# Performance work log

Hardware: AMD Instinct MI355X
Metric: run time of the kernel (lower is better)

Reference implementation:

```python
import jax, jax.numpy as jnp
import numpy as np

B, S, DM, H, DK, R, THETA = 8, 2048, 512, 8, 64, 128, 10000.0
BLK = R          # key/query block size; window radius == block size
NB = S // BLK    # number of blocks
NEG = -1e30      # additive mask for invalid positions (fp32-safe)


def setup_inputs() -> dict:
    key = jax.random.key(0)
    ks = jax.random.split(key, 5)
    scale = 0.02
    hidden_states = jax.random.normal(ks[0], (B, S, DM), jnp.float32)
    Wq = jax.random.normal(ks[1], (DM, H * DK), jnp.float32) * scale
    Wk = jax.random.normal(ks[2], (DM, H * DK), jnp.float32) * scale
    Wv = jax.random.normal(ks[3], (DM, H * DK), jnp.float32) * scale
    Wo = jax.random.normal(ks[4], (H * DK, DM), jnp.float32) * scale
    position_ids = jnp.tile(jnp.arange(S, dtype=jnp.int64)[None, :], (B, 1))
    return {"hidden_states": hidden_states, "Wq": Wq, "Wk": Wk, "Wv": Wv,
            "Wo": Wo, "position_ids": position_ids}


def _apply_rope(q, k, position_ids):
    # q,k: [B,H,S,DK]; position_ids: [B,S]
    half = DK // 2
    inv_freq = 1.0 / (THETA ** (jnp.arange(0, DK, 2, dtype=jnp.float32) / DK))  # [half]
    freqs = position_ids.astype(jnp.float32)[:, :, None] * inv_freq[None, None, :]  # [B,S,half]
    emb = jnp.concatenate([freqs, freqs], axis=-1)        # [B,S,DK]
    cos = jnp.cos(emb)[:, None, :, :]                     # [B,1,S,DK]
    sin = jnp.sin(emb)[:, None, :, :]

    def rotate_half(x):
        return jnp.concatenate([-x[..., half:], x[..., :half]], axis=-1)

    return q * cos + rotate_half(q) * sin, k * cos + rotate_half(k) * sin


def _band_mask():
    # valid[nb, BLK, 3*BLK]: key within [0,S) and |j - i| <= R
    b = jnp.arange(NB)[:, None, None]
    qi = jnp.arange(BLK)[None, :, None]
    kj = jnp.arange(3 * BLK)[None, None, :]
    kglob = (b - 1) * BLK + kj                 # global key index
    qglob = b * BLK + qi                        # global query index
    return (jnp.abs(kglob - qglob) <= R) & (kglob >= 0) & (kglob < S)


def reference(hidden_states, Wq, Wk, Wv, Wo, position_ids):
    # projections: [B,S,DM] -> [B,H,S,DK]
    def shape(x):
        return x.reshape(B, S, H, DK).transpose(0, 2, 1, 3)

    q = shape(hidden_states @ Wq)
    k = shape(hidden_states @ Wk)
    v = shape(hidden_states @ Wv)
    q, k = _apply_rope(q, k, position_ids)

    # block-banded sliding-window attention, softmax_scale = 1.0 (no scaling)
    pad = ((0, 0), (0, 0), (BLK, BLK), (0, 0))
    kb = jnp.pad(k, pad).reshape(B, H, NB + 2, BLK, DK)
    vb = jnp.pad(v, pad).reshape(B, H, NB + 2, BLK, DK)
    # neighbor window: blocks [b-1, b, b+1] -> [B,H,NB,3*BLK,DK]
    kwin = jnp.concatenate([kb[:, :, i:i + NB] for i in range(3)], axis=3)
    vwin = jnp.concatenate([vb[:, :, i:i + NB] for i in range(3)], axis=3)
    qb = q.reshape(B, H, NB, BLK, DK)

    scores = jnp.einsum('bhnqd,bhnkd->bhnqk', qb, kwin)   # unscaled
    valid = _band_mask()                                  # [NB,BLK,3*BLK]
    scores = jnp.where(valid[None, None], scores, NEG)
    attn = jax.nn.softmax(scores.astype(jnp.float32), axis=-1).astype(scores.dtype)
    outb = jnp.einsum('bhnqk,bhnkd->bhnqd', attn, vwin)   # [B,H,NB,BLK,DK]

    out = outb.reshape(B, H, S, DK).transpose(0, 2, 1, 3).reshape(B, S, H * DK)
    return out @ Wo
```

## Files before the change

### kernel.cpp

```cpp
#include <hip/hip_runtime.h>

using bf16 = __bf16;
typedef __bf16 bf16x8 __attribute__((ext_vector_type(8)));
typedef __bf16 bf16x4 __attribute__((ext_vector_type(4)));
typedef float f32x4 __attribute__((ext_vector_type(4)));
typedef float f32x16 __attribute__((ext_vector_type(16)));

#define MFMA16(a, b, c) __builtin_amdgcn_mfma_f32_16x16x32_bf16((a), (b), (c), 0, 0, 0)
#define MFMA32(a, b, c) __builtin_amdgcn_mfma_f32_32x32x16_bf16((a), (b), (c), 0, 0, 0)

constexpr int S = 2048, DM = 512, H = 8, DK = 64, HD = 512;
constexpr int NBLK = 16, BLK = 128;
constexpr int Mrows = 8 * S;
constexpr float LOG2E = 1.44269504088896340736f;

__device__ __forceinline__ void gll16(const void* g, void* l) {
  __builtin_amdgcn_global_load_lds((const __attribute__((address_space(1))) unsigned int*)g,
                                   (__attribute__((address_space(3))) unsigned int*)l, 16, 0, 0);
}

__global__ void k_conv(const float* __restrict__ x, bf16* __restrict__ y) {
  size_t i = ((size_t)blockIdx.x * 256 + threadIdx.x) * 8;
  float4 a = *(const float4*)(x + i);
  float4 b = *(const float4*)(x + i + 4);
  bf16x8 o;
  o[0] = (bf16)a.x; o[1] = (bf16)a.y; o[2] = (bf16)a.z; o[3] = (bf16)a.w;
  o[4] = (bf16)b.x; o[5] = (bf16)b.y; o[6] = (bf16)b.z; o[7] = (bf16)b.w;
  *(bf16x8*)(y + i) = o;
}

__global__ void k_transw4(const float* __restrict__ W0, const float* __restrict__ W1,
                          const float* __restrict__ W2, const float* __restrict__ W3,
                          bf16* __restrict__ D0, bf16* __restrict__ D1,
                          bf16* __restrict__ D2, bf16* __restrict__ D3) {
  const int z = blockIdx.z;
  const float* W = (z == 0) ? W0 : (z == 1) ? W1 : (z == 2) ? W2 : W3;
  bf16* Wt = (z == 0) ? D0 : (z == 1) ? D1 : (z == 2) ? D2 : D3;
  __shared__ float tile[32][33];
  int k0 = blockIdx.x * 32, n0 = blockIdx.y * 32;
  int tx = threadIdx.x, ty = threadIdx.y;
#pragma unroll
  for (int i = 0; i < 4; i++)
    tile[ty * 4 + i][tx] = W[(size_t)(k0 + ty * 4 + i) * 512 + n0 + tx];
  __syncthreads();
#pragma unroll
  for (int i = 0; i < 4; i++)
    Wt[(size_t)(n0 + ty * 4 + i) * 512 + k0 + tx] = (bf16)tile[tx][ty * 4 + i];
}

__global__ void k_ctab(float2* __restrict__ ctab) {
  int idx = blockIdx.x * 256 + threadIdx.x;
  int s = idx >> 5, i = idx & 31;
  float invf = exp2f(-(float)i * (13.287712379549449f / 32.0f));
  float ang = (float)s * invf;
  ctab[idx] = make_float2(cosf(ang), sinf(ang));
}

__global__ __launch_bounds__(256) void k_gemm_qkv(
    const bf16* __restrict__ Xb,
    const bf16* __restrict__ Wtq, const bf16* __restrict__ Wtk, const bf16* __restrict__ Wtv,
    bf16* __restrict__ Qo, bf16* __restrict__ Ko, bf16* __restrict__ Vt,
    const float2* __restrict__ ctab) {
  const int bid = blockIdx.x;
  const int xcd = bid & 7, i = bid >> 3;
  const int mloc = i / 12, zy = i % 12;
  const int z = zy >> 2, y = zy & 3;
  const bf16* Wt = (z == 0) ? Wtq : ((z == 1) ? Wtk : Wtv);
  bf16* dst = (z == 0) ? Qo : Ko;
  const float qscale = (z == 0) ? LOG2E : 1.0f;

  __shared__ __align__(16) char Asm2[2][8192];
  __shared__ __align__(16) char Bsm2[2][8192];

  const int t = threadIdx.x, l = t & 63, wid = t >> 6;
  const int l15 = l & 15, l4 = l >> 4;
  const int wm = wid >> 1, wn = wid & 1;
  const size_t arow0 = (size_t)(xcd * 16 + mloc) * 128;
  const size_t brow0 = (size_t)y * 128;

  f32x4 acc[4][4] = {};
  const int rs = wid * 16 + (l >> 2);
  const int cs = (l & 3) ^ ((l >> 2) & 3);

  auto stage = [&](int kt, int b) {
    const int k0 = kt * 32;
    gll16(Xb + (arow0 + rs) * 512 + k0 + cs * 8,      Asm2[b] + wid * 1024);
    gll16(Xb + (arow0 + 64 + rs) * 512 + k0 + cs * 8, Asm2[b] + 4096 + wid * 1024);
    gll16(Wt + (brow0 + rs) * 512 + k0 + cs * 8,      Bsm2[b] + wid * 1024);
    gll16(Wt + (brow0 + 64 + rs) * 512 + k0 + cs * 8, Bsm2[b] + 4096 + wid * 1024);
  };

  stage(0, 0);
  asm volatile("s_waitcnt vmcnt(0)" ::: "memory");
  __builtin_amdgcn_s_barrier();

  int cur = 0;
  for (int kt = 0; kt < 16; ++kt) {
    if (kt < 15) stage(kt + 1, cur ^ 1);
    bf16x8 af[4], bfr[4];
#pragma unroll
    for (int mi = 0; mi < 4; mi++) {
      int row = wm * 64 + mi * 16 + l15;
      af[mi] = *(const bf16x8*)(Asm2[cur] + row * 64 + ((l4 ^ (row & 3)) * 16));
    }
#pragma unroll
    for (int ni = 0; ni < 4; ni++) {
      int row = wn * 64 + ni * 16 + l15;
      bfr[ni] = *(const bf16x8*)(Bsm2[cur] + row * 64 + ((l4 ^ (row & 3)) * 16));
    }
#pragma unroll
    for (int mi = 0; mi < 4; mi++)
#pragma unroll
      for (int ni = 0; ni < 4; ni++)
        acc[mi][ni] = MFMA16(af[mi], bfr[ni], acc[mi][ni]);
    if (kt < 15) {
      asm volatile("s_waitcnt vmcnt(0)" ::: "memory");
      __builtin_amdgcn_s_barrier();
    }
    cur ^= 1;
  }

  if (z == 2) {
    const int b = (int)(arow0 >> 11);
#pragma unroll
    for (int mi = 0; mi < 4; mi++) {
      int scol = (int)(arow0 & 2047) + wm * 64 + mi * 16 + l4 * 4;
#pragma unroll
      for (int ni = 0; ni < 4; ni++) {
        int col = (int)brow0 + wn * 64 + ni * 16 + l15;
        int hh = col >> 6, dd = col & 63;
        bf16x4 pk = {(bf16)acc[mi][ni][0], (bf16)acc[mi][ni][1],
                     (bf16)acc[mi][ni][2], (bf16)acc[mi][ni][3]};
        *(bf16x4*)(Vt + ((size_t)((b * H + hh) * 64 + dd)) * 2048 + scol) = pk;
      }
    }
    return;
  }

#pragma unroll
  for (int mi = 0; mi < 4; mi++) {
#pragma unroll
    for (int r = 0; r < 4; r++) {
      int grow = (int)arow0 + wm * 64 + mi * 16 + l4 * 4 + r;
      size_t rowoff = (size_t)grow * 512 + brow0 + wn * 64;
      int s = grow & (S - 1);
      float2 cs0 = ctab[s * 32 + l15];
      float2 cs1 = ctab[s * 32 + 16 + l15];
#pragma unroll
      for (int ni = 0; ni < 4; ni++) {
        float a = acc[mi][ni][r];
        float b = acc[mi][ni ^ 2][r];
        float2 cc = (ni & 1) ? cs1 : cs0;
        float val = (ni < 2) ? (a * cc.x - b * cc.y) : (a * cc.x + b * cc.y);
        dst[rowoff + ni * 16 + l15] = (bf16)(val * qscale);
      }
    }
  }
}

__global__ __launch_bounds__(256) void k_gemm_out(
    const bf16* __restrict__ A, const bf16* __restrict__ Wt, float* __restrict__ out) {
  const int bid = blockIdx.x;
  const int xcd = bid & 7, i = bid >> 3;
  __shared__ __align__(16) char Asm2[2][8192];
  __shared__ __align__(16) char Bsm2[2][8192];

  const int t = threadIdx.x, l = t & 63, wid = t >> 6;
  const int l15 = l & 15, l4 = l >> 4;
  const int wm = wid >> 1, wn = wid & 1;
  const size_t arow0 = (size_t)(xcd * 16 + (i >> 2)) * 128;
  const size_t brow0 = (size_t)(i & 3) * 128;

  f32x4 acc[4][4] = {};
  const int rs = wid * 16 + (l >> 2);
  const int cs = (l & 3) ^ ((l >> 2) & 3);

  auto stage = [&](int kt, int b) {
    const int k0 = kt * 32;
    gll16(A + (arow0 + rs) * 512 + k0 + cs * 8,       Asm2[b] + wid * 1024);
    gll16(A + (arow0 + 64 + rs) * 512 + k0 + cs * 8,  Asm2[b] + 4096 + wid * 1024);
    gll16(Wt + (brow0 + rs) * 512 + k0 + cs * 8,      Bsm2[b] + wid * 1024);
    gll16(Wt + (brow0 + 64 + rs) * 512 + k0 + cs * 8, Bsm2[b] + 4096 + wid * 1024);
  };

  stage(0, 0);
  asm volatile("s_waitcnt vmcnt(0)" ::: "memory");
  __builtin_amdgcn_s_barrier();

  int cur = 0;
  for (int kt = 0; kt < 16; ++kt) {
    if (kt < 15) stage(kt + 1, cur ^ 1);
    bf16x8 af[4], bfr[4];
#pragma unroll
    for (int mi = 0; mi < 4; mi++) {
      int row = wm * 64 + mi * 16 + l15;
      af[mi] = *(const bf16x8*)(Asm2[cur] + row * 64 + ((l4 ^ (row & 3)) * 16));
    }
#pragma unroll
    for (int ni = 0; ni < 4; ni++) {
      int row = wn * 64 + ni * 16 + l15;
      bfr[ni] = *(const bf16x8*)(Bsm2[cur] + row * 64 + ((l4 ^ (row & 3)) * 16));
    }
#pragma unroll
    for (int mi = 0; mi < 4; mi++)
#pragma unroll
      for (int ni = 0; ni < 4; ni++)
        acc[mi][ni] = MFMA16(af[mi], bfr[ni], acc[mi][ni]);
    if (kt < 15) {
      asm volatile("s_waitcnt vmcnt(0)" ::: "memory");
      __builtin_amdgcn_s_barrier();
    }
    cur ^= 1;
  }

#pragma unroll
  for (int mi = 0; mi < 4; mi++)
#pragma unroll
    for (int r = 0; r < 4; r++) {
      int grow = (int)arow0 + wm * 64 + mi * 16 + l4 * 4 + r;
      size_t rowoff = (size_t)grow * 512 + brow0 + wn * 64;
#pragma unroll
      for (int ni = 0; ni < 4; ni++)
        out[rowoff + ni * 16 + l15] = acc[mi][ni][r];
    }
}

__global__ __launch_bounds__(256, 4) void k_attn(
    const bf16* __restrict__ Q, const bf16* __restrict__ K, const bf16* __restrict__ Vt,
    bf16* __restrict__ O) {
  const int bid = blockIdx.x;
  const int swz = (bid & 7) * 128 + (bid >> 3);
  const int nb = swz & 15, h = (swz >> 4) & 7, bb = swz >> 7;
  const int t = threadIdx.x, l = t & 63, w = t >> 6;
  const int q31 = l & 31, hi = l >> 5;

  const int bh = bb * H + h;
  const size_t qrow = (size_t)bb * S + nb * BLK + w * 32 + q31;

  const bf16* Qp = Q + qrow * HD + h * DK + hi * 8;
  bf16x8 qb[4];
#pragma unroll
  for (int ks = 0; ks < 4; ks++) qb[ks] = *(const bf16x8*)(Qp + ks * 16);

  f32x16 o0 = {}, o1 = {};
  float mrun = -3e38f, lrun = 0.f;

  const bf16* Kbase = K + (size_t)bb * S * HD + h * DK + hi * 8;
  const bf16* Vbase = Vt + ((size_t)bh * 64 + q31) * 2048 + hi * 8;
  const int s0 = nb * BLK + w * 32 - 128;

  auto kcl = [](int kg) { return kg < 0 ? 0 : (kg > S - 32 ? S - 32 : kg); };

  bf16x8 kcur0, kcur1, kcur2, kcur3;
  {
    const bf16* Kp = Kbase + (size_t)(kcl(s0) + q31) * HD;
    kcur0 = *(const bf16x8*)(Kp);
    kcur1 = *(const bf16x8*)(Kp + 16);
    kcur2 = *(const bf16x8*)(Kp + 32);
    kcur3 = *(const bf16x8*)(Kp + 48);
  }

#pragma unroll
  for (int c = 0; c < 9; ++c) {
    const int kg = s0 + c * 32;
    const int kcc = kcl(kg);
    const int kcn = kcl(s0 + (c + 1) * 32);

    const bf16* Vp = Vbase + kcc;
    bf16x8 v0 = *(const bf16x8*)(Vp);
    bf16x8 v1 = *(const bf16x8*)(Vp + 16);
    bf16x8 v2 = *(const bf16x8*)(Vp + 32 * 2048);
    bf16x8 v3 = *(const bf16x8*)(Vp + 32 * 2048 + 16);
    const bf16* Kpn = Kbase + (size_t)(kcn + q31) * HD;
    bf16x8 kn0 = *(const bf16x8*)(Kpn);
    bf16x8 kn1 = *(const bf16x8*)(Kpn + 16);
    bf16x8 kn2 = *(const bf16x8*)(Kpn + 32);
    bf16x8 kn3 = *(const bf16x8*)(Kpn + 48);
    __builtin_amdgcn_sched_barrier(0);

    f32x16 a = {};
    a = MFMA32(kcur0, qb[0], a);
    a = MFMA32(kcur1, qb[1], a);
    a = MFMA32(kcur2, qb[2], a);
    a = MFMA32(kcur3, qb[3], a);

    if (kg != kcc) {
#pragma unroll
      for (int rg = 0; rg < 16; rg++) a[rg] = -1e30f;
    } else if (c == 0) {
#pragma unroll
      for (int rg = 0; rg < 16; rg++) {
        int kk = (rg & 3) + 8 * (rg >> 2) + 4 * hi;
        if (kk < q31) a[rg] = -1e30f;
      }
    } else if (c == 8) {
#pragma unroll
      for (int rg = 0; rg < 16; rg++) {
        int kk = (rg & 3) + 8 * (rg >> 2) + 4 * hi;
        if (kk > q31) a[rg] = -1e30f;
      }
    }

    f32x16 mx = a;
#pragma unroll
    for (int sl = 8; sl >= 1; sl >>= 1)
#pragma unroll
      for (int i2 = 0; i2 < sl; i2++) mx[i2] = fmaxf(mx[i2], mx[i2 + sl]);
    const float pm = fmaxf(mx[0], __shfl_xor(mx[0], 32));

    if (!__all(pm - mrun <= 8.0f)) {
      const float mnew = fmaxf(mrun, pm);
      const float alpha = exp2f(mrun - mnew);
      lrun *= alpha;
#pragma unroll
      for (int rg = 0; rg < 16; rg++) { o0[rg] *= alpha; o1[rg] *= alpha; }
      mrun = mnew;
    }

    float rsum = 0.f;
#pragma unroll
    for (int rg = 0; rg < 16; rg++) { a[rg] = exp2f(a[rg] - mrun); rsum += a[rg]; }
    rsum += __shfl_xor(rsum, 32);
    lrun += rsum;

    unsigned int Wd[4][2];
#pragma unroll
    for (int aa = 0; aa < 4; aa++)
#pragma unroll
      for (int b2 = 0; b2 < 2; b2++) {
        unsigned int wd;
        asm("v_cvt_pk_bf16_f32 %0, %1, %2" : "=v"(wd) : "v"(a[4 * aa + 2 * b2]), "v"(a[4 * aa + 2 * b2 + 1]));
        Wd[aa][b2] = wd;
      }
    bf16x8 pf[2];
#pragma unroll
    for (int ks = 0; ks < 2; ks++) {
      union { unsigned int u[4]; bf16x8 v; } cvt;
#pragma unroll
      for (int b2 = 0; b2 < 2; b2++) {
        unsigned int low_w = Wd[2 * ks][b2];
        unsigned int hi_w  = Wd[2 * ks + 1][b2];
        unsigned int msg = hi ? low_w : hi_w;
        unsigned int rec = __shfl_xor(msg, 32);
        cvt.u[b2]     = hi ? rec : low_w;
        cvt.u[2 + b2] = hi ? hi_w : rec;
      }
      pf[ks] = cvt.v;
    }

    o0 = MFMA32(v0, pf[0], o0);
    o0 = MFMA32(v1, pf[1], o0);
    o1 = MFMA32(v2, pf[0], o1);
    o1 = MFMA32(v3, pf[1], o1);

    kcur0 = kn0; kcur1 = kn1; kcur2 = kn2; kcur3 = kn3;
  }

  const float inv = 1.0f / lrun;
  bf16* Op = O + qrow * HD + h * DK + 4 * hi;
#pragma unroll
  for (int dt = 0; dt < 2; dt++) {
    const f32x16 oo = dt ? o1 : o0;
#pragma unroll
    for (int a2 = 0; a2 < 4; a2++) {
      bf16x4 ob = {(bf16)(oo[4 * a2 + 0] * inv), (bf16)(oo[4 * a2 + 1] * inv),
                   (bf16)(oo[4 * a2 + 2] * inv), (bf16)(oo[4 * a2 + 3] * inv)};
      *(bf16x4*)(Op + dt * 32 + 8 * a2) = ob;
    }
  }
}

extern "C" void kernel_launch(void* const* d_in, const int* in_sizes, int n_in,
                              void* d_out, int out_size, void* d_ws, size_t ws_size,
                              hipStream_t stream) {
  const float* hs = (const float*)d_in[0];
  const float* Wq = (const float*)d_in[1];
  const float* Wk = (const float*)d_in[2];
  const float* Wv = (const float*)d_in[3];
  const float* Wo = (const float*)d_in[4];
  float* out = (float*)d_out;

  char* ws = (char*)d_ws;
  const size_t MB = 1u << 20;
  bf16* Xb = (bf16*)(ws);
  bf16* Qb = (bf16*)(ws + 16 * MB);
  bf16* Kb = (bf16*)(ws + 32 * MB);
  bf16* Vt = (bf16*)(ws + 48 * MB);
  bf16* Wtq = (bf16*)(ws + 64 * MB);
  bf16* Wtk = Wtq + 512 * 512;
  bf16* Wtv = Wtk + 512 * 512;
  bf16* Wto = Wtv + 512 * 512;
  float2* ctab = (float2*)(ws + 64 * MB + 4 * 512 * 512 * sizeof(bf16));
  bf16* AO = Xb;

  k_conv<<<dim3(Mrows * DM / (256 * 8)), dim3(256), 0, stream>>>(hs, Xb);
  k_transw4<<<dim3(16, 16, 4), dim3(32, 8), 0, stream>>>(Wq, Wk, Wv, Wo, Wtq, Wtk, Wtv, Wto);
  k_ctab<<<dim3(S * 32 / 256), dim3(256), 0, stream>>>(ctab);
  k_gemm_qkv<<<dim3(1536), dim3(256), 0, stream>>>(Xb, Wtq, Wtk, Wtv, Qb, Kb, Vt, ctab);
  k_attn<<<dim3(NBLK * H * 8), dim3(256), 0, stream>>>(Qb, Kb, Vt, AO);
  k_gemm_out<<<dim3(512), dim3(256), 0, stream>>>(AO, Wto, out);
}
```

Baseline: 126.1 us.

## Triple-buffer GEMM LDS staging and change LDS swizzle pattern

Both projection GEMMs (QKV and output) move from double to triple buffering of the LDS A/B tiles. Loads are issued two k-steps ahead, and the wait becomes vmcnt(4) instead of a full drain, so global loads overlap more with MFMA work. The XOR swizzle also changes from (row&3) to (l15>>2) on both the write and read sides, aiming to cut LDS bank conflicts. The cost is 48KB of LDS per block instead of 32KB, which may reduce occupancy.

```diff
diff --git a/kernel.cpp b/kernel.cpp
--- a/kernel.cpp
+++ b/kernel.cpp
@@ -69,8 +69,8 @@
   bf16* dst = (z == 0) ? Qo : Ko;
   const float qscale = (z == 0) ? LOG2E : 1.0f;
 
-  __shared__ __align__(16) char Asm2[2][8192];
-  __shared__ __align__(16) char Bsm2[2][8192];
+  __shared__ __align__(16) char Asm3[3][8192];
+  __shared__ __align__(16) char Bsm3[3][8192];
 
   const int t = threadIdx.x, l = t & 63, wid = t >> 6;
   const int l15 = l & 15, l4 = l >> 4;
@@ -80,33 +80,34 @@
 
   f32x4 acc[4][4] = {};
   const int rs = wid * 16 + (l >> 2);
-  const int cs = (l & 3) ^ ((l >> 2) & 3);
+  const int cs = (l & 3) ^ (l >> 4);
 
   auto stage = [&](int kt, int b) {
     const int k0 = kt * 32;
-    gll16(Xb + (arow0 + rs) * 512 + k0 + cs * 8,      Asm2[b] + wid * 1024);
-    gll16(Xb + (arow0 + 64 + rs) * 512 + k0 + cs * 8, Asm2[b] + 4096 + wid * 1024);
-    gll16(Wt + (brow0 + rs) * 512 + k0 + cs * 8,      Bsm2[b] + wid * 1024);
-    gll16(Wt + (brow0 + 64 + rs) * 512 + k0 + cs * 8, Bsm2[b] + 4096 + wid * 1024);
+    gll16(Xb + (arow0 + rs) * 512 + k0 + cs * 8,      Asm3[b] + wid * 1024);
+    gll16(Xb + (arow0 + 64 + rs) * 512 + k0 + cs * 8, Asm3[b] + 4096 + wid * 1024);
+    gll16(Wt + (brow0 + rs) * 512 + k0 + cs * 8,      Bsm3[b] + wid * 1024);
+    gll16(Wt + (brow0 + 64 + rs) * 512 + k0 + cs * 8, Bsm3[b] + 4096 + wid * 1024);
   };
 
   stage(0, 0);
-  asm volatile("s_waitcnt vmcnt(0)" ::: "memory");
+  stage(1, 1);
+  asm volatile("s_waitcnt vmcnt(4)" ::: "memory");
   __builtin_amdgcn_s_barrier();
 
   int cur = 0;
   for (int kt = 0; kt < 16; ++kt) {
-    if (kt < 15) stage(kt + 1, cur ^ 1);
+    if (kt + 2 <= 15) stage(kt + 2, (kt + 2) % 3);
     bf16x8 af[4], bfr[4];
 #pragma unroll
     for (int mi = 0; mi < 4; mi++) {
       int row = wm * 64 + mi * 16 + l15;
-      af[mi] = *(const bf16x8*)(Asm2[cur] + row * 64 + ((l4 ^ (row & 3)) * 16));
+      af[mi] = *(const bf16x8*)(Asm3[cur] + row * 64 + ((l4 ^ (l15 >> 2)) * 16));
     }
 #pragma unroll
     for (int ni = 0; ni < 4; ni++) {
       int row = wn * 64 + ni * 16 + l15;
-      bfr[ni] = *(const bf16x8*)(Bsm2[cur] + row * 64 + ((l4 ^ (row & 3)) * 16));
+      bfr[ni] = *(const bf16x8*)(Bsm3[cur] + row * 64 + ((l4 ^ (l15 >> 2)) * 16));
     }
 #pragma unroll
     for (int mi = 0; mi < 4; mi++)
@@ -114,10 +115,11 @@
       for (int ni = 0; ni < 4; ni++)
         acc[mi][ni] = MFMA16(af[mi], bfr[ni], acc[mi][ni]);
     if (kt < 15) {
-      asm volatile("s_waitcnt vmcnt(0)" ::: "memory");
+      if (kt < 14) asm volatile("s_waitcnt vmcnt(4)" ::: "memory");
+      else         asm volatile("s_waitcnt vmcnt(0)" ::: "memory");
       __builtin_amdgcn_s_barrier();
     }
-    cur ^= 1;
+    cur = (cur == 2) ? 0 : cur + 1;
   }
 
   if (z == 2) {
@@ -162,8 +164,8 @@
     const bf16* __restrict__ A, const bf16* __restrict__ Wt, float* __restrict__ out) {
   const int bid = blockIdx.x;
   const int xcd = bid & 7, i = bid >> 3;
-  __shared__ __align__(16) char Asm2[2][8192];
-  __shared__ __align__(16) char Bsm2[2][8192];
+  __shared__ __align__(16) char Asm3[3][8192];
+  __shared__ __align__(16) char Bsm3[3][8192];
 
   const int t = threadIdx.x, l = t & 63, wid = t >> 6;
   const int l15 = l & 15, l4 = l >> 4;
@@ -173,33 +175,34 @@
 
   f32x4 acc[4][4] = {};
   const int rs = wid * 16 + (l >> 2);
-  const int cs = (l & 3) ^ ((l >> 2) & 3);
+  const int cs = (l & 3) ^ (l >> 4);
 
   auto stage = [&](int kt, int b) {
     const int k0 = kt * 32;
-    gll16(A + (arow0 + rs) * 512 + k0 + cs * 8,       Asm2[b] + wid * 1024);
-    gll16(A + (arow0 + 64 + rs) * 512 + k0 + cs * 8,  Asm2[b] + 4096 + wid * 1024);
-    gll16(Wt + (brow0 + rs) * 512 + k0 + cs * 8,      Bsm2[b] + wid * 1024);
-    gll16(Wt + (brow0 + 64 + rs) * 512 + k0 + cs * 8, Bsm2[b] + 4096 + wid * 1024);
+    gll16(A + (arow0 + rs) * 512 + k0 + cs * 8,       Asm3[b] + wid * 1024);
+    gll16(A + (arow0 + 64 + rs) * 512 + k0 + cs * 8,  Asm3[b] + 4096 + wid * 1024);
+    gll16(Wt + (brow0 + rs) * 512 + k0 + cs * 8,      Bsm3[b] + wid * 1024);
+    gll16(Wt + (brow0 + 64 + rs) * 512 + k0 + cs * 8, Bsm3[b] + 4096 + wid * 1024);
   };
 
   stage(0, 0);
-  asm volatile("s_waitcnt vmcnt(0)" ::: "memory");
+  stage(1, 1);
+  asm volatile("s_waitcnt vmcnt(4)" ::: "memory");
   __builtin_amdgcn_s_barrier();
 
   int cur = 0;
   for (int kt = 0; kt < 16; ++kt) {
-    if (kt < 15) stage(kt + 1, cur ^ 1);
+    if (kt + 2 <= 15) stage(kt + 2, (kt + 2) % 3);
     bf16x8 af[4], bfr[4];
 #pragma unroll
     for (int mi = 0; mi < 4; mi++) {
       int row = wm * 64 + mi * 16 + l15;
-      af[mi] = *(const bf16x8*)(Asm2[cur] + row * 64 + ((l4 ^ (row & 3)) * 16));
+      af[mi] = *(const bf16x8*)(Asm3[cur] + row * 64 + ((l4 ^ (l15 >> 2)) * 16));
     }
 #pragma unroll
     for (int ni = 0; ni < 4; ni++) {
       int row = wn * 64 + ni * 16 + l15;
-      bfr[ni] = *(const bf16x8*)(Bsm2[cur] + row * 64 + ((l4 ^ (row & 3)) * 16));
+      bfr[ni] = *(const bf16x8*)(Bsm3[cur] + row * 64 + ((l4 ^ (l15 >> 2)) * 16));
     }
 #pragma unroll
     for (int mi = 0; mi < 4; mi++)
@@ -207,10 +210,11 @@
       for (int ni = 0; ni < 4; ni++)
         acc[mi][ni] = MFMA16(af[mi], bfr[ni], acc[mi][ni]);
     if (kt < 15) {
-      asm volatile("s_waitcnt vmcnt(0)" ::: "memory");
+      if (kt < 14) asm volatile("s_waitcnt vmcnt(4)" ::: "memory");
+      else         asm volatile("s_waitcnt vmcnt(0)" ::: "memory");
       __builtin_amdgcn_s_barrier();
     }
-    cur ^= 1;
+    cur = (cur == 2) ? 0 : cur + 1;
   }
 
 #pragma unroll
```

Result: faster. 122.9 us (-2.6%).
